# Optimization experiments

Hardware: AMD Instinct MI355X
Metric: run time of the kernel (lower is better)

## Reference

```python
import jax, jax.numpy as jnp
import numpy as np

B, N, D, H, T = 2048, 128, 256, 8, 64
HD = D // H
TANH_C = 10.0
MASK_PENALTY = 1e9


def setup_inputs() -> dict:
    key = jax.random.key(0)
    ks = jax.random.split(key, 16)
    s = 1.0 / np.sqrt(D).astype(np.float32)
    w = lambda k: jax.random.normal(k, (D, D), jnp.float32) * s
    return {
        'node_emb': jax.random.normal(ks[0], (B, N, D), jnp.float32),
        'graph_emb': jax.random.normal(ks[1], (B, D), jnp.float32),
        'W_target': w(ks[2]), 'W_global': w(ks[3]),
        'W_K1': w(ks[4]), 'W_K2': w(ks[5]),
        'W_Q': w(ks[6]), 'W_V': w(ks[7]),
        'Wq_m': w(ks[8]), 'Wk_m': w(ks[9]), 'Wv_m': w(ks[10]), 'Wo_m': w(ks[11]),
        'targets': jax.random.randint(ks[12], (T, B), 0, N, jnp.int32),
        'masks': jax.random.randint(ks[13], (T, B, N), 0, 2, jnp.int32),
    }


def _mha(q, k, v, Wq, Wk, Wv, Wo):
    # q: [B,1,D]; k,v: [B,N,D]. Standard multi-head attention (glimpse).
    qh = (q @ Wq.T).reshape(B, 1, H, HD).transpose(0, 2, 1, 3)   # [B,H,1,HD]
    kh = (k @ Wk.T).reshape(B, N, H, HD).transpose(0, 2, 1, 3)   # [B,H,N,HD]
    vh = (v @ Wv.T).reshape(B, N, H, HD).transpose(0, 2, 1, 3)
    scores = jnp.einsum('bhqd,bhnd->bhqn', qh, kh) / np.sqrt(HD).astype(np.float32)
    attn = jax.nn.softmax(scores, axis=-1)
    out = jnp.einsum('bhqn,bhnd->bhqd', attn, vh)                # [B,H,1,HD]
    out = out.transpose(0, 2, 1, 3).reshape(B, 1, D)
    return out @ Wo.T


def reference(node_emb, graph_emb, W_target, W_global, W_K1, W_K2, W_Q, W_V,
              Wq_m, Wk_m, Wv_m, Wo_m, targets, masks):
    # Step-invariant projections (embeddings fixed across decode steps here).
    keys = node_emb @ W_K1.T      # [B,N,D]
    vals = node_emb @ W_V.T       # [B,N,D]
    key2 = node_emb @ W_K2.T      # [B,N,D]
    g_ctx = graph_emb @ W_global.T  # [B,D]
    inv_sqrt_d = np.float32(1.0 / np.sqrt(D))

    def step(ll, tm):
        tgt, mask = tm  # tgt:[B] int32, mask:[B,N] int32
        tgt_emb = jnp.take_along_axis(node_emb, tgt[:, None, None], axis=1)[:, 0, :]  # [B,D]
        context = (tgt_emb @ W_target.T + g_ctx)[:, None, :]      # [B,1,D]
        glimpse = _mha(context, keys, vals, Wq_m, Wk_m, Wv_m, Wo_m)  # [B,1,D]
        query = glimpse @ W_Q.T                                    # [B,1,D]
        logits = jnp.einsum('bqd,bnd->bn', query, key2) * inv_sqrt_d  # [B,N]
        logits = TANH_C * jnp.tanh(logits) - mask.astype(jnp.float32) * MASK_PENALTY
        log_p = jax.nn.log_softmax(logits, axis=1)
        actions = jnp.argmax(log_p, axis=1)                        # greedy TopKSampler
        ll = ll + jnp.take_along_axis(log_p, actions[:, None], axis=1)[:, 0]
        return ll, None

    ll, _ = jax.lax.scan(step, jnp.zeros(B, jnp.float32), (targets, masks))
    return ll
```

## Files before the change

kernel.cpp:

```cpp
#include <hip/hip_runtime.h>
#include <hip/hip_bf16.h>

#define BB 2048
#define NN 128
#define DD 256
#define HH 8
#define TT 64

typedef __bf16 bf16x8 __attribute__((ext_vector_type(8)));
typedef float f32x4 __attribute__((ext_vector_type(4)));

static __device__ __forceinline__ f32x4 mfma16(bf16x8 a, bf16x8 b, f32x4 c) {
  return __builtin_amdgcn_mfma_f32_16x16x32_bf16(a, b, c, 0, 0, 0);
}

static __device__ __forceinline__ f32x4 zero4() {
  f32x4 z = {0.f, 0.f, 0.f, 0.f};
  return z;
}

static __device__ __forceinline__ bf16x8 cvt8(const float* p) {
  const float4 x0 = *(const float4*)p;
  const float4 x1 = *(const float4*)(p + 4);
  bf16x8 r;
  r[0] = (__bf16)x0.x; r[1] = (__bf16)x0.y; r[2] = (__bf16)x0.z; r[3] = (__bf16)x0.w;
  r[4] = (__bf16)x1.x; r[5] = (__bf16)x1.y; r[6] = (__bf16)x1.z; r[7] = (__bf16)x1.w;
  return r;
}

__global__ void fold1(const float* __restrict__ Wq_m, const float* __restrict__ W_target,
                      const float* __restrict__ W_global, const float* __restrict__ Wk_m,
                      const float* __restrict__ W_K1, const float* __restrict__ Wv_m,
                      const float* __restrict__ W_V, const float* __restrict__ W_Q,
                      const float* __restrict__ Wo_m,
                      __bf16* __restrict__ WTQ, float* __restrict__ WGQT,
                      __bf16* __restrict__ WKH, __bf16* __restrict__ WVH,
                      float* __restrict__ WQO) {
  const int p = blockIdx.x >> 8;
  const int i = blockIdx.x & 255;
  const int t = threadIdx.x;
  __shared__ float arow[256];
  const float* A;
  const float* Bm;
  if (p == 0)      { A = Wq_m; Bm = W_target; }
  else if (p == 1) { A = Wq_m; Bm = W_global; }
  else if (p == 2) { A = Wk_m; Bm = W_K1; }
  else if (p == 3) { A = Wv_m; Bm = W_V; }
  else             { A = W_Q;  Bm = Wo_m; }
  arow[t] = A[i * 256 + t];
  __syncthreads();
  float acc = 0.f;
  for (int k = 0; k < 256; ++k) acc = fmaf(arow[k], Bm[k * 256 + t], acc);
  if (p == 0)      WTQ[i * 256 + t] = (__bf16)acc;
  else if (p == 1) WGQT[t * 256 + i] = acc;
  else if (p == 2) WKH[i * 256 + t] = (__bf16)acc;
  else if (p == 3) WVH[i * 256 + t] = (__bf16)acc;
  else             WQO[i * 256 + t] = acc;
}

__global__ void fold2(const float* __restrict__ WQO, const float* __restrict__ W_K2,
                      __bf16* __restrict__ WZL) {
  const int j = blockIdx.x;
  const int t = threadIdx.x;
  __shared__ float col[256];
  col[t] = W_K2[t * 256 + j];
  __syncthreads();
  float acc = 0.f;
  for (int d = 0; d < 256; ++d) acc = fmaf(WQO[d * 256 + t], col[d], acc);
  WZL[j * 256 + t] = (__bf16)acc;
}

__global__ void gq_kernel(const float* __restrict__ ge, const float* __restrict__ WGQT,
                          float* __restrict__ GQ) {
  const int b = blockIdx.x;
  const int t = threadIdx.x;
  __shared__ float g[256];
  g[t] = ge[b * 256 + t];
  __syncthreads();
  float acc = 0.f;
  for (int j = 0; j < 256; ++j) acc = fmaf(WGQT[j * 256 + t], g[j], acc);
  GQ[b * 256 + t] = acc;
}

__global__ __launch_bounds__(256, 2)
void glimpse_kernel(const float* __restrict__ E, const int* __restrict__ tg,
                    const __bf16* __restrict__ WTQ, const __bf16* __restrict__ WKH,
                    const __bf16* __restrict__ WVH, const float* __restrict__ GQ,
                    __bf16* __restrict__ HO) {
  const int b = blockIdx.x;
  const int tid = threadIdx.x;
  const int w = tid >> 6;
  const int l = tid & 63;
  const int lr = l & 15;
  const int lg = l >> 4;

  __shared__ __bf16 Qs[64 * 264];
  __shared__ __bf16 KHs[128 * 40];
  __shared__ __bf16 VTs[32 * 136];
  __shared__ __bf16 Ps[64 * 136];
  __shared__ int tgs[64];

  if (tid < 64) tgs[tid] = tg[tid * BB + b];
  __syncthreads();

  const float* Eb = E + (size_t)b * NN * DD;

  {
    f32x4 acc[4][4];
#pragma unroll
    for (int mf = 0; mf < 4; ++mf)
#pragma unroll
      for (int nf = 0; nf < 4; ++nf) acc[mf][nf] = zero4();
    const int n0 = w * 64;
    for (int kk = 0; kk < 8; ++kk) {
      bf16x8 aF[4], bF[4];
#pragma unroll
      for (int mf = 0; mf < 4; ++mf) {
        const int node = tgs[mf * 16 + lr];
        aF[mf] = cvt8(Eb + node * DD + kk * 32 + lg * 8);
      }
#pragma unroll
      for (int nf = 0; nf < 4; ++nf)
        bF[nf] = *(const bf16x8*)(WTQ + (size_t)(n0 + nf * 16 + lr) * DD + kk * 32 + lg * 8);
#pragma unroll
      for (int mf = 0; mf < 4; ++mf)
#pragma unroll
        for (int nf = 0; nf < 4; ++nf) acc[mf][nf] = mfma16(aF[mf], bF[nf], acc[mf][nf]);
    }
#pragma unroll
    for (int nf = 0; nf < 4; ++nf) {
      const int col = n0 + nf * 16 + lr;
      const float g = GQ[b * DD + col];
#pragma unroll
      for (int mf = 0; mf < 4; ++mf)
#pragma unroll
        for (int r = 0; r < 4; ++r)
          Qs[(mf * 16 + lg * 4 + r) * 264 + col] = (__bf16)(acc[mf][nf][r] + g);
    }
  }

  for (int h = 0; h < HH; ++h) {
    __syncthreads();
    {
      f32x4 ak[2][2], av[2][2];
#pragma unroll
      for (int mf = 0; mf < 2; ++mf)
#pragma unroll
        for (int nf = 0; nf < 2; ++nf) { ak[mf][nf] = zero4(); av[mf][nf] = zero4(); }
      for (int kk = 0; kk < 8; ++kk) {
        bf16x8 aF[2], bK[2], bV[2];
#pragma unroll
        for (int mf = 0; mf < 2; ++mf)
          aF[mf] = cvt8(Eb + (w * 32 + mf * 16 + lr) * DD + kk * 32 + lg * 8);
#pragma unroll
        for (int nf = 0; nf < 2; ++nf) {
          const size_t wo = (size_t)(h * 32 + nf * 16 + lr) * DD + kk * 32 + lg * 8;
          bK[nf] = *(const bf16x8*)(WKH + wo);
          bV[nf] = *(const bf16x8*)(WVH + wo);
        }
#pragma unroll
        for (int mf = 0; mf < 2; ++mf)
#pragma unroll
          for (int nf = 0; nf < 2; ++nf) {
            ak[mf][nf] = mfma16(aF[mf], bK[nf], ak[mf][nf]);
            av[mf][nf] = mfma16(aF[mf], bV[nf], av[mf][nf]);
          }
      }
#pragma unroll
      for (int mf = 0; mf < 2; ++mf)
#pragma unroll
        for (int nf = 0; nf < 2; ++nf)
#pragma unroll
          for (int r = 0; r < 4; ++r) {
            const int node = w * 32 + mf * 16 + lg * 4 + r;
            const int d = nf * 16 + lr;
            KHs[node * 40 + d] = (__bf16)ak[mf][nf][r];
            VTs[d * 136 + node] = (__bf16)av[mf][nf][r];
          }
    }
    __syncthreads();
    {
      const bf16x8 aq = *(const bf16x8*)&Qs[(w * 16 + lr) * 264 + h * 32 + lg * 8];
      f32x4 s[8];
#pragma unroll
      for (int nf = 0; nf < 8; ++nf)
        s[nf] = mfma16(aq, *(const bf16x8*)&KHs[(nf * 16 + lr) * 40 + lg * 8], zero4());

      float mx[4] = {-1e30f, -1e30f, -1e30f, -1e30f};
#pragma unroll
      for (int nf = 0; nf < 8; ++nf)
#pragma unroll
        for (int r = 0; r < 4; ++r) mx[r] = fmaxf(mx[r], s[nf][r]);
#pragma unroll
      for (int mk = 1; mk <= 8; mk <<= 1)
#pragma unroll
        for (int r = 0; r < 4; ++r) mx[r] = fmaxf(mx[r], __shfl_xor(mx[r], mk));

      float ev[8][4];
      float sm[4] = {0.f, 0.f, 0.f, 0.f};
#pragma unroll
      for (int nf = 0; nf < 8; ++nf)
#pragma unroll
        for (int r = 0; r < 4; ++r) {
          ev[nf][r] = __expf((s[nf][r] - mx[r]) * 0.17677669529663687f);
          sm[r] += ev[nf][r];
        }
#pragma unroll
      for (int mk = 1; mk <= 8; mk <<= 1)
#pragma unroll
        for (int r = 0; r < 4; ++r) sm[r] += __shfl_xor(sm[r], mk);

#pragma unroll
      for (int nf = 0; nf < 8; ++nf)
#pragma unroll
        for (int r = 0; r < 4; ++r)
          Ps[(w * 16 + lg * 4 + r) * 136 + nf * 16 + lr] = (__bf16)ev[nf][r];

      f32x4 o[2] = {zero4(), zero4()};
#pragma unroll
      for (int kk = 0; kk < 4; ++kk) {
        const bf16x8 ap = *(const bf16x8*)&Ps[(w * 16 + lr) * 136 + kk * 32 + lg * 8];
#pragma unroll
        for (int nf2 = 0; nf2 < 2; ++nf2)
          o[nf2] = mfma16(ap, *(const bf16x8*)&VTs[(nf2 * 16 + lr) * 136 + kk * 32 + lg * 8],
                          o[nf2]);
      }
      float inv[4];
#pragma unroll
      for (int r = 0; r < 4; ++r) inv[r] = 1.f / sm[r];
#pragma unroll
      for (int nf2 = 0; nf2 < 2; ++nf2)
#pragma unroll
        for (int r = 0; r < 4; ++r) {
          const int t = w * 16 + lg * 4 + r;
          HO[((size_t)t * BB + b) * DD + h * 32 + nf2 * 16 + lr] =
              (__bf16)(o[nf2][r] * inv[r]);
        }
    }
  }
}

__global__ __launch_bounds__(256, 2)
void logits_kernel(const float* __restrict__ E, const __bf16* __restrict__ HO,
                   const __bf16* __restrict__ WZL, const int* __restrict__ MK,
                   float* __restrict__ out) {
  const int b = blockIdx.x;
  const int tid = threadIdx.x;
  const int w = tid >> 6;
  const int l = tid & 63;
  const int lr = l & 15;
  const int lg = l >> 4;

  __shared__ __bf16 HOs[64 * 264];
  __shared__ __bf16 Zs[64 * 264];
  __shared__ float red[4];

#pragma unroll
  for (int it = 0; it < 8; ++it) {
    const int lin = it * 256 + tid;
    const int tr = lin >> 5;
    const int c8 = lin & 31;
    *(bf16x8*)&HOs[tr * 264 + c8 * 8] =
        *(const bf16x8*)(HO + ((size_t)tr * BB + b) * DD + c8 * 8);
  }
  __syncthreads();

  {
    f32x4 acc[4][4];
#pragma unroll
    for (int mf = 0; mf < 4; ++mf)
#pragma unroll
      for (int nf = 0; nf < 4; ++nf) acc[mf][nf] = zero4();
    for (int kk = 0; kk < 8; ++kk) {
      bf16x8 aF[4], bF[4];
#pragma unroll
      for (int mf = 0; mf < 4; ++mf)
        aF[mf] = *(const bf16x8*)&HOs[(mf * 16 + lr) * 264 + kk * 32 + lg * 8];
#pragma unroll
      for (int nf = 0; nf < 4; ++nf)
        bF[nf] = *(const bf16x8*)(WZL + (size_t)(w * 64 + nf * 16 + lr) * DD + kk * 32 + lg * 8);
#pragma unroll
      for (int mf = 0; mf < 4; ++mf)
#pragma unroll
        for (int nf = 0; nf < 4; ++nf) acc[mf][nf] = mfma16(aF[mf], bF[nf], acc[mf][nf]);
    }
#pragma unroll
    for (int mf = 0; mf < 4; ++mf)
#pragma unroll
      for (int nf = 0; nf < 4; ++nf)
#pragma unroll
        for (int r = 0; r < 4; ++r)
          Zs[(mf * 16 + lg * 4 + r) * 264 + w * 64 + nf * 16 + lr] = (__bf16)acc[mf][nf][r];
  }
  __syncthreads();

  {
    const float* Eb = E + (size_t)b * NN * DD;
    f32x4 sa[8];
#pragma unroll
    for (int nf = 0; nf < 8; ++nf) sa[nf] = zero4();
    for (int kk = 0; kk < 8; ++kk) {
      const bf16x8 az = *(const bf16x8*)&Zs[(w * 16 + lr) * 264 + kk * 32 + lg * 8];
#pragma unroll
      for (int nf = 0; nf < 8; ++nf) {
        const bf16x8 be = cvt8(Eb + (nf * 16 + lr) * DD + kk * 32 + lg * 8);
        sa[nf] = mfma16(az, be, sa[nf]);
      }
    }
    float xv[8][4];
    float mx[4] = {-3e38f, -3e38f, -3e38f, -3e38f};
    float sm[4] = {0.f, 0.f, 0.f, 0.f};
#pragma unroll
    for (int nf = 0; nf < 8; ++nf)
#pragma unroll
      for (int r = 0; r < 4; ++r) {
        const int t = w * 16 + lg * 4 + r;
        const int n = nf * 16 + lr;
        const int m = MK[((size_t)t * BB + b) * NN + n];
        const float x = 10.f * tanhf(sa[nf][r] * 0.0625f) - (float)m * 1e9f;
        xv[nf][r] = x;
        mx[r] = fmaxf(mx[r], x);
      }
#pragma unroll
    for (int mk = 1; mk <= 8; mk <<= 1)
#pragma unroll
      for (int r = 0; r < 4; ++r) mx[r] = fmaxf(mx[r], __shfl_xor(mx[r], mk));
#pragma unroll
    for (int nf = 0; nf < 8; ++nf)
#pragma unroll
      for (int r = 0; r < 4; ++r) sm[r] += __expf(xv[nf][r] - mx[r]);
#pragma unroll
    for (int mk = 1; mk <= 8; mk <<= 1)
#pragma unroll
      for (int r = 0; r < 4; ++r) sm[r] += __shfl_xor(sm[r], mk);

    float part = logf(sm[0]) + logf(sm[1]) + logf(sm[2]) + logf(sm[3]);
    part += __shfl_xor(part, 16);
    part += __shfl_xor(part, 32);
    if (l == 0) red[w] = part;
  }
  __syncthreads();
  if (tid == 0) out[b] = -(red[0] + red[1] + red[2] + red[3]);
}

extern "C" void kernel_launch(void* const* d_in, const int* in_sizes, int n_in,
                              void* d_out, int out_size, void* d_ws, size_t ws_size,
                              hipStream_t stream) {
  (void)in_sizes; (void)n_in; (void)out_size; (void)ws_size;
  const float* node_emb  = (const float*)d_in[0];
  const float* graph_emb = (const float*)d_in[1];
  const float* W_target  = (const float*)d_in[2];
  const float* W_global  = (const float*)d_in[3];
  const float* W_K1      = (const float*)d_in[4];
  const float* W_K2      = (const float*)d_in[5];
  const float* W_Q       = (const float*)d_in[6];
  const float* W_V       = (const float*)d_in[7];
  const float* Wq_m      = (const float*)d_in[8];
  const float* Wk_m      = (const float*)d_in[9];
  const float* Wv_m      = (const float*)d_in[10];
  const float* Wo_m      = (const float*)d_in[11];
  const int* targets     = (const int*)d_in[12];
  const int* masks       = (const int*)d_in[13];

  char* p = (char*)d_ws;
  __bf16* HO  = (__bf16*)p; p += (size_t)TT * BB * DD * 2;
  __bf16* WTQ = (__bf16*)p; p += 256 * 256 * 2;
  __bf16* WKH = (__bf16*)p; p += 256 * 256 * 2;
  __bf16* WVH = (__bf16*)p; p += 256 * 256 * 2;
  __bf16* WZL = (__bf16*)p; p += 256 * 256 * 2;
  float* WGQT = (float*)p;  p += 256 * 256 * 4;
  float* WQO  = (float*)p;  p += 256 * 256 * 4;
  float* GQ   = (float*)p;  p += (size_t)BB * DD * 4;

  fold1<<<1280, 256, 0, stream>>>(Wq_m, W_target, W_global, Wk_m, W_K1, Wv_m, W_V, W_Q, Wo_m,
                                  WTQ, WGQT, WKH, WVH, WQO);
  fold2<<<256, 256, 0, stream>>>(WQO, W_K2, WZL);
  gq_kernel<<<BB, 256, 0, stream>>>(graph_emb, WGQT, GQ);
  glimpse_kernel<<<BB, 256, 0, stream>>>(node_emb, targets, WTQ, WKH, WVH, GQ, HO);
  logits_kernel<<<BB, 256, 0, stream>>>(node_emb, HO, WZL, masks, (float*)d_out);
}
```

Baseline: 616.5 us.

## Split glimpse kernel across head pairs and use fast tanh in logits

The glimpse kernel now launches four blocks per batch element, each handling two heads (64 columns). Each block computes its slice of Q, K and V in one pass and drops the per-head sync loop. This raises parallelism and shrinks shared memory per block. The cost is that the node embedding rows are loaded and converted four times per batch element instead of once. Separately, tanhf in the logits kernel is replaced by an exp/rcp formula, which is cheaper but slightly less accurate.

```diff
diff --git a/kernel.cpp b/kernel.cpp
--- a/kernel.cpp
+++ b/kernel.cpp
@@ -26,6 +26,11 @@
   r[0] = (__bf16)x0.x; r[1] = (__bf16)x0.y; r[2] = (__bf16)x0.z; r[3] = (__bf16)x0.w;
   r[4] = (__bf16)x1.x; r[5] = (__bf16)x1.y; r[6] = (__bf16)x1.z; r[7] = (__bf16)x1.w;
   return r;
+}
+
+static __device__ __forceinline__ float fast_tanh10(float y) {
+  const float e = __expf(2.f * y);
+  return 10.f - 20.f * __builtin_amdgcn_rcpf(1.f + e);
 }
 
 __global__ void fold1(const float* __restrict__ Wq_m, const float* __restrict__ W_target,
@@ -83,20 +88,21 @@
 }
 
 __global__ __launch_bounds__(256, 2)
-void glimpse_kernel(const float* __restrict__ E, const int* __restrict__ tg,
-                    const __bf16* __restrict__ WTQ, const __bf16* __restrict__ WKH,
-                    const __bf16* __restrict__ WVH, const float* __restrict__ GQ,
-                    __bf16* __restrict__ HO) {
-  const int b = blockIdx.x;
+void glimpse2_kernel(const float* __restrict__ E, const int* __restrict__ tg,
+                     const __bf16* __restrict__ WTQ, const __bf16* __restrict__ WKH,
+                     const __bf16* __restrict__ WVH, const float* __restrict__ GQ,
+                     __bf16* __restrict__ HO) {
+  const int b = blockIdx.x >> 2;
+  const int c0 = (blockIdx.x & 3) * 64;
   const int tid = threadIdx.x;
   const int w = tid >> 6;
   const int l = tid & 63;
   const int lr = l & 15;
   const int lg = l >> 4;
 
-  __shared__ __bf16 Qs[64 * 264];
-  __shared__ __bf16 KHs[128 * 40];
-  __shared__ __bf16 VTs[32 * 136];
+  __shared__ __bf16 Qs[64 * 72];
+  __shared__ __bf16 KHs[128 * 72];
+  __shared__ __bf16 VTs[64 * 136];
   __shared__ __bf16 Ps[64 * 136];
   __shared__ int tgs[64];
 
@@ -106,137 +112,123 @@
   const float* Eb = E + (size_t)b * NN * DD;
 
   {
-    f32x4 acc[4][4];
-#pragma unroll
-    for (int mf = 0; mf < 4; ++mf)
-#pragma unroll
-      for (int nf = 0; nf < 4; ++nf) acc[mf][nf] = zero4();
-    const int n0 = w * 64;
+    f32x4 acc[4] = {zero4(), zero4(), zero4(), zero4()};
+    const int node = tgs[w * 16 + lr];
     for (int kk = 0; kk < 8; ++kk) {
-      bf16x8 aF[4], bF[4];
-#pragma unroll
-      for (int mf = 0; mf < 4; ++mf) {
-        const int node = tgs[mf * 16 + lr];
-        aF[mf] = cvt8(Eb + node * DD + kk * 32 + lg * 8);
-      }
-#pragma unroll
-      for (int nf = 0; nf < 4; ++nf)
-        bF[nf] = *(const bf16x8*)(WTQ + (size_t)(n0 + nf * 16 + lr) * DD + kk * 32 + lg * 8);
-#pragma unroll
-      for (int mf = 0; mf < 4; ++mf)
-#pragma unroll
-        for (int nf = 0; nf < 4; ++nf) acc[mf][nf] = mfma16(aF[mf], bF[nf], acc[mf][nf]);
+      const bf16x8 aF = cvt8(Eb + node * DD + kk * 32 + lg * 8);
+#pragma unroll
+      for (int nf = 0; nf < 4; ++nf) {
+        const bf16x8 bF =
+            *(const bf16x8*)(WTQ + (size_t)(c0 + nf * 16 + lr) * DD + kk * 32 + lg * 8);
+        acc[nf] = mfma16(aF, bF, acc[nf]);
+      }
     }
 #pragma unroll
     for (int nf = 0; nf < 4; ++nf) {
-      const int col = n0 + nf * 16 + lr;
-      const float g = GQ[b * DD + col];
-#pragma unroll
-      for (int mf = 0; mf < 4; ++mf)
-#pragma unroll
-        for (int r = 0; r < 4; ++r)
-          Qs[(mf * 16 + lg * 4 + r) * 264 + col] = (__bf16)(acc[mf][nf][r] + g);
-    }
-  }
-
-  for (int h = 0; h < HH; ++h) {
-    __syncthreads();
-    {
-      f32x4 ak[2][2], av[2][2];
+      const int cl = nf * 16 + lr;
+      const float g = GQ[b * DD + c0 + cl];
+#pragma unroll
+      for (int r = 0; r < 4; ++r)
+        Qs[(w * 16 + lg * 4 + r) * 72 + cl] = (__bf16)(acc[nf][r] + g);
+    }
+  }
+
+  {
+    f32x4 acc[2][8];
+#pragma unroll
+    for (int mf = 0; mf < 2; ++mf)
+#pragma unroll
+      for (int nf = 0; nf < 8; ++nf) acc[mf][nf] = zero4();
+    for (int kk = 0; kk < 8; ++kk) {
+      bf16x8 aF[2], bF[8];
 #pragma unroll
       for (int mf = 0; mf < 2; ++mf)
-#pragma unroll
-        for (int nf = 0; nf < 2; ++nf) { ak[mf][nf] = zero4(); av[mf][nf] = zero4(); }
-      for (int kk = 0; kk < 8; ++kk) {
-        bf16x8 aF[2], bK[2], bV[2];
-#pragma unroll
-        for (int mf = 0; mf < 2; ++mf)
-          aF[mf] = cvt8(Eb + (w * 32 + mf * 16 + lr) * DD + kk * 32 + lg * 8);
-#pragma unroll
-        for (int nf = 0; nf < 2; ++nf) {
-          const size_t wo = (size_t)(h * 32 + nf * 16 + lr) * DD + kk * 32 + lg * 8;
-          bK[nf] = *(const bf16x8*)(WKH + wo);
-          bV[nf] = *(const bf16x8*)(WVH + wo);
-        }
-#pragma unroll
-        for (int mf = 0; mf < 2; ++mf)
-#pragma unroll
-          for (int nf = 0; nf < 2; ++nf) {
-            ak[mf][nf] = mfma16(aF[mf], bK[nf], ak[mf][nf]);
-            av[mf][nf] = mfma16(aF[mf], bV[nf], av[mf][nf]);
-          }
+        aF[mf] = cvt8(Eb + (w * 32 + mf * 16 + lr) * DD + kk * 32 + lg * 8);
+#pragma unroll
+      for (int nf = 0; nf < 4; ++nf) {
+        const size_t wo = (size_t)(c0 + nf * 16 + lr) * DD + kk * 32 + lg * 8;
+        bF[nf] = *(const bf16x8*)(WKH + wo);
+        bF[nf + 4] = *(const bf16x8*)(WVH + wo);
       }
 #pragma unroll
       for (int mf = 0; mf < 2; ++mf)
 #pragma unroll
-        for (int nf = 0; nf < 2; ++nf)
-#pragma unroll
-          for (int r = 0; r < 4; ++r) {
-            const int node = w * 32 + mf * 16 + lg * 4 + r;
-            const int d = nf * 16 + lr;
-            KHs[node * 40 + d] = (__bf16)ak[mf][nf][r];
-            VTs[d * 136 + node] = (__bf16)av[mf][nf][r];
-          }
-    }
-    __syncthreads();
-    {
-      const bf16x8 aq = *(const bf16x8*)&Qs[(w * 16 + lr) * 264 + h * 32 + lg * 8];
-      f32x4 s[8];
-#pragma unroll
-      for (int nf = 0; nf < 8; ++nf)
-        s[nf] = mfma16(aq, *(const bf16x8*)&KHs[(nf * 16 + lr) * 40 + lg * 8], zero4());
-
-      float mx[4] = {-1e30f, -1e30f, -1e30f, -1e30f};
-#pragma unroll
-      for (int nf = 0; nf < 8; ++nf)
-#pragma unroll
-        for (int r = 0; r < 4; ++r) mx[r] = fmaxf(mx[r], s[nf][r]);
-#pragma unroll
-      for (int mk = 1; mk <= 8; mk <<= 1)
-#pragma unroll
-        for (int r = 0; r < 4; ++r) mx[r] = fmaxf(mx[r], __shfl_xor(mx[r], mk));
-
-      float ev[8][4];
-      float sm[4] = {0.f, 0.f, 0.f, 0.f};
-#pragma unroll
-      for (int nf = 0; nf < 8; ++nf)
-#pragma unroll
-        for (int r = 0; r < 4; ++r) {
-          ev[nf][r] = __expf((s[nf][r] - mx[r]) * 0.17677669529663687f);
-          sm[r] += ev[nf][r];
-        }
-#pragma unroll
-      for (int mk = 1; mk <= 8; mk <<= 1)
-#pragma unroll
-        for (int r = 0; r < 4; ++r) sm[r] += __shfl_xor(sm[r], mk);
-
-#pragma unroll
-      for (int nf = 0; nf < 8; ++nf)
-#pragma unroll
-        for (int r = 0; r < 4; ++r)
-          Ps[(w * 16 + lg * 4 + r) * 136 + nf * 16 + lr] = (__bf16)ev[nf][r];
-
-      f32x4 o[2] = {zero4(), zero4()};
-#pragma unroll
-      for (int kk = 0; kk < 4; ++kk) {
-        const bf16x8 ap = *(const bf16x8*)&Ps[(w * 16 + lr) * 136 + kk * 32 + lg * 8];
-#pragma unroll
-        for (int nf2 = 0; nf2 < 2; ++nf2)
-          o[nf2] = mfma16(ap, *(const bf16x8*)&VTs[(nf2 * 16 + lr) * 136 + kk * 32 + lg * 8],
-                          o[nf2]);
-      }
-      float inv[4];
-#pragma unroll
-      for (int r = 0; r < 4; ++r) inv[r] = 1.f / sm[r];
+        for (int nf = 0; nf < 8; ++nf) acc[mf][nf] = mfma16(aF[mf], bF[nf], acc[mf][nf]);
+    }
+#pragma unroll
+    for (int mf = 0; mf < 2; ++mf)
+#pragma unroll
+      for (int r = 0; r < 4; ++r) {
+        const int node = w * 32 + mf * 16 + lg * 4 + r;
+#pragma unroll
+        for (int nf = 0; nf < 4; ++nf)
+          KHs[node * 72 + nf * 16 + lr] = (__bf16)acc[mf][nf][r];
+#pragma unroll
+        for (int nf = 0; nf < 4; ++nf)
+          VTs[(nf * 16 + lr) * 136 + node] = (__bf16)acc[mf][nf + 4][r];
+      }
+  }
+  __syncthreads();
+
+#pragma unroll
+  for (int h = 0; h < 2; ++h) {
+    const bf16x8 aq = *(const bf16x8*)&Qs[(w * 16 + lr) * 72 + h * 32 + lg * 8];
+    f32x4 s[8];
+#pragma unroll
+    for (int nf = 0; nf < 8; ++nf)
+      s[nf] = mfma16(aq, *(const bf16x8*)&KHs[(nf * 16 + lr) * 72 + h * 32 + lg * 8], zero4());
+
+    float mx[4] = {-1e30f, -1e30f, -1e30f, -1e30f};
+#pragma unroll
+    for (int nf = 0; nf < 8; ++nf)
+#pragma unroll
+      for (int r = 0; r < 4; ++r) mx[r] = fmaxf(mx[r], s[nf][r]);
+#pragma unroll
+    for (int mk = 1; mk <= 8; mk <<= 1)
+#pragma unroll
+      for (int r = 0; r < 4; ++r) mx[r] = fmaxf(mx[r], __shfl_xor(mx[r], mk));
+
+    float ev[8][4];
+    float sm[4] = {0.f, 0.f, 0.f, 0.f};
+#pragma unroll
+    for (int nf = 0; nf < 8; ++nf)
+#pragma unroll
+      for (int r = 0; r < 4; ++r) {
+        ev[nf][r] = __expf((s[nf][r] - mx[r]) * 0.17677669529663687f);
+        sm[r] += ev[nf][r];
+      }
+#pragma unroll
+    for (int mk = 1; mk <= 8; mk <<= 1)
+#pragma unroll
+      for (int r = 0; r < 4; ++r) sm[r] += __shfl_xor(sm[r], mk);
+
+#pragma unroll
+    for (int nf = 0; nf < 8; ++nf)
+#pragma unroll
+      for (int r = 0; r < 4; ++r)
+        Ps[(w * 16 + lg * 4 + r) * 136 + nf * 16 + lr] = (__bf16)ev[nf][r];
+
+    f32x4 o[2] = {zero4(), zero4()};
+#pragma unroll
+    for (int kk = 0; kk < 4; ++kk) {
+      const bf16x8 ap = *(const bf16x8*)&Ps[(w * 16 + lr) * 136 + kk * 32 + lg * 8];
 #pragma unroll
       for (int nf2 = 0; nf2 < 2; ++nf2)
-#pragma unroll
-        for (int r = 0; r < 4; ++r) {
-          const int t = w * 16 + lg * 4 + r;
-          HO[((size_t)t * BB + b) * DD + h * 32 + nf2 * 16 + lr] =
-              (__bf16)(o[nf2][r] * inv[r]);
-        }
-    }
+        o[nf2] = mfma16(
+            ap, *(const bf16x8*)&VTs[(h * 32 + nf2 * 16 + lr) * 136 + kk * 32 + lg * 8],
+            o[nf2]);
+    }
+    float inv[4];
+#pragma unroll
+    for (int r = 0; r < 4; ++r) inv[r] = 1.f / sm[r];
+#pragma unroll
+    for (int nf2 = 0; nf2 < 2; ++nf2)
+#pragma unroll
+      for (int r = 0; r < 4; ++r) {
+        const int t = w * 16 + lg * 4 + r;
+        HO[((size_t)t * BB + b) * DD + c0 + h * 32 + nf2 * 16 + lr] =
+            (__bf16)(o[nf2][r] * inv[r]);
+      }
   }
 }
 
@@ -317,7 +309,7 @@
         const int t = w * 16 + lg * 4 + r;
         const int n = nf * 16 + lr;
         const int m = MK[((size_t)t * BB + b) * NN + n];
-        const float x = 10.f * tanhf(sa[nf][r] * 0.0625f) - (float)m * 1e9f;
+        const float x = fast_tanh10(sa[nf][r] * 0.0625f) - (float)m * 1e9f;
         xv[nf][r] = x;
         mx[r] = fmaxf(mx[r], x);
       }
@@ -376,6 +368,6 @@
                                   WTQ, WGQT, WKH, WVH, WQO);
   fold2<<<256, 256, 0, stream>>>(WQO, W_K2, WZL);
   gq_kernel<<<BB, 256, 0, stream>>>(graph_emb, WGQT, GQ);
-  glimpse_kernel<<<BB, 256, 0, stream>>>(node_emb, targets, WTQ, WKH, WVH, GQ, HO);
+  glimpse2_kernel<<<BB * 4, 256, 0, stream>>>(node_emb, targets, WTQ, WKH, WVH, GQ, HO);
   logits_kernel<<<BB, 256, 0, stream>>>(node_emb, HO, WZL, masks, (float*)d_out);
 }
```

Measured after the change: 751.9 us. 1.22x slower.

## Split K/V projection into its own kernel and fuse attention with logits

Applied to the files above, without the earlier changes.

Moves the per-batch key/value head projections into a separate kernel. It stages node embeddings in LDS as bf16 once and writes K and V-transposed for all heads to global memory. The attention and logits stages merge into one kernel that reads K and V from global and keeps head outputs in LDS and registers, so the large HO intermediate round trip goes away. It also replaces tanhf with an exp plus reciprocal formulation. The cost is writing and reading KH and VT (two B×N×D bf16 buffers), a larger LDS tile in the KV kernel that may lower occupancy, and slightly different tanh accuracy.

```diff
diff --git a/kernel.cpp b/kernel.cpp
--- a/kernel.cpp
+++ b/kernel.cpp
@@ -26,6 +26,11 @@
   r[0] = (__bf16)x0.x; r[1] = (__bf16)x0.y; r[2] = (__bf16)x0.z; r[3] = (__bf16)x0.w;
   r[4] = (__bf16)x1.x; r[5] = (__bf16)x1.y; r[6] = (__bf16)x1.z; r[7] = (__bf16)x1.w;
   return r;
+}
+
+static __device__ __forceinline__ float fast_tanh10(float y) {
+  const float e = __expf(2.f * y);
+  return 10.f - 20.f * __builtin_amdgcn_rcpf(1.f + e);
 }
 
 __global__ void fold1(const float* __restrict__ Wq_m, const float* __restrict__ W_target,
@@ -82,168 +87,90 @@
   GQ[b * 256 + t] = acc;
 }
 
-__global__ __launch_bounds__(256, 2)
-void glimpse_kernel(const float* __restrict__ E, const int* __restrict__ tg,
-                    const __bf16* __restrict__ WTQ, const __bf16* __restrict__ WKH,
-                    const __bf16* __restrict__ WVH, const float* __restrict__ GQ,
-                    __bf16* __restrict__ HO) {
+__global__ __launch_bounds__(256)
+void kv_kernel(const float* __restrict__ E, const __bf16* __restrict__ WKH,
+               const __bf16* __restrict__ WVH, __bf16* __restrict__ KH,
+               __bf16* __restrict__ VT) {
   const int b = blockIdx.x;
   const int tid = threadIdx.x;
   const int w = tid >> 6;
   const int l = tid & 63;
   const int lr = l & 15;
   const int lg = l >> 4;
-
-  __shared__ __bf16 Qs[64 * 264];
-  __shared__ __bf16 KHs[128 * 40];
-  __shared__ __bf16 VTs[32 * 136];
-  __shared__ __bf16 Ps[64 * 136];
-  __shared__ int tgs[64];
-
-  if (tid < 64) tgs[tid] = tg[tid * BB + b];
-  __syncthreads();
-
+  __shared__ __bf16 Es[128 * 264];
   const float* Eb = E + (size_t)b * NN * DD;
-
-  {
-    f32x4 acc[4][4];
+  for (int c = tid; c < 4096; c += 256) {
+    const int row = c >> 5;
+    const int c8 = c & 31;
+    *(bf16x8*)&Es[row * 264 + c8 * 8] = cvt8(Eb + row * 256 + c8 * 8);
+  }
+  __syncthreads();
+
+  {
+    f32x4 acc[8][4];
+#pragma unroll
+    for (int mf = 0; mf < 8; ++mf)
+#pragma unroll
+      for (int nf = 0; nf < 4; ++nf) acc[mf][nf] = zero4();
+    for (int kk = 0; kk < 8; ++kk) {
+      bf16x8 aF[8], bF[4];
+#pragma unroll
+      for (int mf = 0; mf < 8; ++mf)
+        aF[mf] = *(const bf16x8*)&Es[(mf * 16 + lr) * 264 + kk * 32 + lg * 8];
+#pragma unroll
+      for (int nf = 0; nf < 4; ++nf)
+        bF[nf] = *(const bf16x8*)(WKH + (size_t)(w * 64 + nf * 16 + lr) * DD + kk * 32 + lg * 8);
+#pragma unroll
+      for (int mf = 0; mf < 8; ++mf)
+#pragma unroll
+        for (int nf = 0; nf < 4; ++nf) acc[mf][nf] = mfma16(aF[mf], bF[nf], acc[mf][nf]);
+    }
+    __bf16* KHb = KH + (size_t)b * NN * DD;
+#pragma unroll
+    for (int mf = 0; mf < 8; ++mf)
+#pragma unroll
+      for (int nf = 0; nf < 4; ++nf)
+#pragma unroll
+        for (int r = 0; r < 4; ++r)
+          KHb[(mf * 16 + lg * 4 + r) * DD + w * 64 + nf * 16 + lr] = (__bf16)acc[mf][nf][r];
+  }
+
+  {
+    f32x4 acc[4][8];
 #pragma unroll
     for (int mf = 0; mf < 4; ++mf)
 #pragma unroll
-      for (int nf = 0; nf < 4; ++nf) acc[mf][nf] = zero4();
-    const int n0 = w * 64;
-    for (int kk = 0; kk < 8; ++kk) {
-      bf16x8 aF[4], bF[4];
-#pragma unroll
-      for (int mf = 0; mf < 4; ++mf) {
-        const int node = tgs[mf * 16 + lr];
-        aF[mf] = cvt8(Eb + node * DD + kk * 32 + lg * 8);
-      }
-#pragma unroll
-      for (int nf = 0; nf < 4; ++nf)
-        bF[nf] = *(const bf16x8*)(WTQ + (size_t)(n0 + nf * 16 + lr) * DD + kk * 32 + lg * 8);
-#pragma unroll
-      for (int mf = 0; mf < 4; ++mf)
-#pragma unroll
-        for (int nf = 0; nf < 4; ++nf) acc[mf][nf] = mfma16(aF[mf], bF[nf], acc[mf][nf]);
-    }
-#pragma unroll
-    for (int nf = 0; nf < 4; ++nf) {
-      const int col = n0 + nf * 16 + lr;
-      const float g = GQ[b * DD + col];
-#pragma unroll
-      for (int mf = 0; mf < 4; ++mf)
+      for (int nf = 0; nf < 8; ++nf) acc[mf][nf] = zero4();
+    for (int kk = 0; kk < 8; ++kk) {
+      bf16x8 aF[4], bF[8];
+#pragma unroll
+      for (int mf = 0; mf < 4; ++mf)
+        aF[mf] = *(const bf16x8*)(WVH + (size_t)(w * 64 + mf * 16 + lr) * DD + kk * 32 + lg * 8);
+#pragma unroll
+      for (int nf = 0; nf < 8; ++nf)
+        bF[nf] = *(const bf16x8*)&Es[(nf * 16 + lr) * 264 + kk * 32 + lg * 8];
+#pragma unroll
+      for (int mf = 0; mf < 4; ++mf)
+#pragma unroll
+        for (int nf = 0; nf < 8; ++nf) acc[mf][nf] = mfma16(aF[mf], bF[nf], acc[mf][nf]);
+    }
+    __bf16* VTb = VT + (size_t)b * DD * NN;
+#pragma unroll
+    for (int mf = 0; mf < 4; ++mf)
+#pragma unroll
+      for (int nf = 0; nf < 8; ++nf)
 #pragma unroll
         for (int r = 0; r < 4; ++r)
-          Qs[(mf * 16 + lg * 4 + r) * 264 + col] = (__bf16)(acc[mf][nf][r] + g);
-    }
-  }
-
-  for (int h = 0; h < HH; ++h) {
-    __syncthreads();
-    {
-      f32x4 ak[2][2], av[2][2];
-#pragma unroll
-      for (int mf = 0; mf < 2; ++mf)
-#pragma unroll
-        for (int nf = 0; nf < 2; ++nf) { ak[mf][nf] = zero4(); av[mf][nf] = zero4(); }
-      for (int kk = 0; kk < 8; ++kk) {
-        bf16x8 aF[2], bK[2], bV[2];
-#pragma unroll
-        for (int mf = 0; mf < 2; ++mf)
-          aF[mf] = cvt8(Eb + (w * 32 + mf * 16 + lr) * DD + kk * 32 + lg * 8);
-#pragma unroll
-        for (int nf = 0; nf < 2; ++nf) {
-          const size_t wo = (size_t)(h * 32 + nf * 16 + lr) * DD + kk * 32 + lg * 8;
-          bK[nf] = *(const bf16x8*)(WKH + wo);
-          bV[nf] = *(const bf16x8*)(WVH + wo);
-        }
-#pragma unroll
-        for (int mf = 0; mf < 2; ++mf)
-#pragma unroll
-          for (int nf = 0; nf < 2; ++nf) {
-            ak[mf][nf] = mfma16(aF[mf], bK[nf], ak[mf][nf]);
-            av[mf][nf] = mfma16(aF[mf], bV[nf], av[mf][nf]);
-          }
-      }
-#pragma unroll
-      for (int mf = 0; mf < 2; ++mf)
-#pragma unroll
-        for (int nf = 0; nf < 2; ++nf)
-#pragma unroll
-          for (int r = 0; r < 4; ++r) {
-            const int node = w * 32 + mf * 16 + lg * 4 + r;
-            const int d = nf * 16 + lr;
-            KHs[node * 40 + d] = (__bf16)ak[mf][nf][r];
-            VTs[d * 136 + node] = (__bf16)av[mf][nf][r];
-          }
-    }
-    __syncthreads();
-    {
-      const bf16x8 aq = *(const bf16x8*)&Qs[(w * 16 + lr) * 264 + h * 32 + lg * 8];
-      f32x4 s[8];
-#pragma unroll
-      for (int nf = 0; nf < 8; ++nf)
-        s[nf] = mfma16(aq, *(const bf16x8*)&KHs[(nf * 16 + lr) * 40 + lg * 8], zero4());
-
-      float mx[4] = {-1e30f, -1e30f, -1e30f, -1e30f};
-#pragma unroll
-      for (int nf = 0; nf < 8; ++nf)
-#pragma unroll
-        for (int r = 0; r < 4; ++r) mx[r] = fmaxf(mx[r], s[nf][r]);
-#pragma unroll
-      for (int mk = 1; mk <= 8; mk <<= 1)
-#pragma unroll
-        for (int r = 0; r < 4; ++r) mx[r] = fmaxf(mx[r], __shfl_xor(mx[r], mk));
-
-      float ev[8][4];
-      float sm[4] = {0.f, 0.f, 0.f, 0.f};
-#pragma unroll
-      for (int nf = 0; nf < 8; ++nf)
-#pragma unroll
-        for (int r = 0; r < 4; ++r) {
-          ev[nf][r] = __expf((s[nf][r] - mx[r]) * 0.17677669529663687f);
-          sm[r] += ev[nf][r];
-        }
-#pragma unroll
-      for (int mk = 1; mk <= 8; mk <<= 1)
-#pragma unroll
-        for (int r = 0; r < 4; ++r) sm[r] += __shfl_xor(sm[r], mk);
-
-#pragma unroll
-      for (int nf = 0; nf < 8; ++nf)
-#pragma unroll
-        for (int r = 0; r < 4; ++r)
-          Ps[(w * 16 + lg * 4 + r) * 136 + nf * 16 + lr] = (__bf16)ev[nf][r];
-
-      f32x4 o[2] = {zero4(), zero4()};
-#pragma unroll
-      for (int kk = 0; kk < 4; ++kk) {
-        const bf16x8 ap = *(const bf16x8*)&Ps[(w * 16 + lr) * 136 + kk * 32 + lg * 8];
-#pragma unroll
-        for (int nf2 = 0; nf2 < 2; ++nf2)
-          o[nf2] = mfma16(ap, *(const bf16x8*)&VTs[(nf2 * 16 + lr) * 136 + kk * 32 + lg * 8],
-                          o[nf2]);
-      }
-      float inv[4];
-#pragma unroll
-      for (int r = 0; r < 4; ++r) inv[r] = 1.f / sm[r];
-#pragma unroll
-      for (int nf2 = 0; nf2 < 2; ++nf2)
-#pragma unroll
-        for (int r = 0; r < 4; ++r) {
-          const int t = w * 16 + lg * 4 + r;
-          HO[((size_t)t * BB + b) * DD + h * 32 + nf2 * 16 + lr] =
-              (__bf16)(o[nf2][r] * inv[r]);
-        }
-    }
-  }
-}
-
-__global__ __launch_bounds__(256, 2)
-void logits_kernel(const float* __restrict__ E, const __bf16* __restrict__ HO,
-                   const __bf16* __restrict__ WZL, const int* __restrict__ MK,
-                   float* __restrict__ out) {
+          VTb[(w * 64 + mf * 16 + lg * 4 + r) * NN + nf * 16 + lr] = (__bf16)acc[mf][nf][r];
+  }
+}
+
+__global__ __launch_bounds__(256)
+void attn_logits_kernel(const float* __restrict__ E, const int* __restrict__ tg,
+                        const __bf16* __restrict__ WTQ, const float* __restrict__ GQ,
+                        const __bf16* __restrict__ KH, const __bf16* __restrict__ VT,
+                        const __bf16* __restrict__ WZL, const int* __restrict__ MK,
+                        float* __restrict__ out) {
   const int b = blockIdx.x;
   const int tid = threadIdx.x;
   const int w = tid >> 6;
@@ -251,59 +178,134 @@
   const int lr = l & 15;
   const int lg = l >> 4;
 
-  __shared__ __bf16 HOs[64 * 264];
-  __shared__ __bf16 Zs[64 * 264];
+  __shared__ __bf16 Qs[64 * 264];
+  __shared__ __bf16 Ps[64 * 136];
   __shared__ float red[4];
 
-#pragma unroll
-  for (int it = 0; it < 8; ++it) {
-    const int lin = it * 256 + tid;
-    const int tr = lin >> 5;
-    const int c8 = lin & 31;
-    *(bf16x8*)&HOs[tr * 264 + c8 * 8] =
-        *(const bf16x8*)(HO + ((size_t)tr * BB + b) * DD + c8 * 8);
-  }
-  __syncthreads();
-
-  {
-    f32x4 acc[4][4];
+  const float* Eb = E + (size_t)b * NN * DD;
+
+  {
+    f32x4 qa[4][4];
 #pragma unroll
     for (int mf = 0; mf < 4; ++mf)
 #pragma unroll
-      for (int nf = 0; nf < 4; ++nf) acc[mf][nf] = zero4();
+      for (int nf = 0; nf < 4; ++nf) qa[mf][nf] = zero4();
+    const int n0 = w * 64;
+    int nd[4];
+#pragma unroll
+    for (int mf = 0; mf < 4; ++mf) nd[mf] = tg[(mf * 16 + lr) * BB + b];
     for (int kk = 0; kk < 8; ++kk) {
       bf16x8 aF[4], bF[4];
 #pragma unroll
       for (int mf = 0; mf < 4; ++mf)
-        aF[mf] = *(const bf16x8*)&HOs[(mf * 16 + lr) * 264 + kk * 32 + lg * 8];
+        aF[mf] = cvt8(Eb + (size_t)nd[mf] * DD + kk * 32 + lg * 8);
 #pragma unroll
       for (int nf = 0; nf < 4; ++nf)
-        bF[nf] = *(const bf16x8*)(WZL + (size_t)(w * 64 + nf * 16 + lr) * DD + kk * 32 + lg * 8);
-#pragma unroll
-      for (int mf = 0; mf < 4; ++mf)
-#pragma unroll
-        for (int nf = 0; nf < 4; ++nf) acc[mf][nf] = mfma16(aF[mf], bF[nf], acc[mf][nf]);
-    }
-#pragma unroll
-    for (int mf = 0; mf < 4; ++mf)
-#pragma unroll
-      for (int nf = 0; nf < 4; ++nf)
+        bF[nf] = *(const bf16x8*)(WTQ + (size_t)(n0 + nf * 16 + lr) * DD + kk * 32 + lg * 8);
+#pragma unroll
+      for (int mf = 0; mf < 4; ++mf)
+#pragma unroll
+        for (int nf = 0; nf < 4; ++nf) qa[mf][nf] = mfma16(aF[mf], bF[nf], qa[mf][nf]);
+    }
+#pragma unroll
+    for (int nf = 0; nf < 4; ++nf) {
+      const int col = n0 + nf * 16 + lr;
+      const float g = GQ[b * DD + col];
+#pragma unroll
+      for (int mf = 0; mf < 4; ++mf)
 #pragma unroll
         for (int r = 0; r < 4; ++r)
-          Zs[(mf * 16 + lg * 4 + r) * 264 + w * 64 + nf * 16 + lr] = (__bf16)acc[mf][nf][r];
-  }
-  __syncthreads();
-
-  {
-    const float* Eb = E + (size_t)b * NN * DD;
+          Qs[(mf * 16 + lg * 4 + r) * 264 + col] = (__bf16)(qa[mf][nf][r] + g);
+    }
+  }
+  __syncthreads();
+
+  const __bf16* KHb = KH + (size_t)b * NN * DD;
+  const __bf16* VTb = VT + (size_t)b * DD * NN;
+  f32x4 hov[16];
+
+#pragma unroll
+  for (int h = 0; h < HH; ++h) {
+    const bf16x8 aq = *(const bf16x8*)&Qs[(w * 16 + lr) * 264 + h * 32 + lg * 8];
+    f32x4 s[8];
+#pragma unroll
+    for (int nf = 0; nf < 8; ++nf)
+      s[nf] = mfma16(aq, *(const bf16x8*)(KHb + (size_t)(nf * 16 + lr) * DD + h * 32 + lg * 8),
+                     zero4());
+
+    float mx[4] = {-1e30f, -1e30f, -1e30f, -1e30f};
+#pragma unroll
+    for (int nf = 0; nf < 8; ++nf)
+#pragma unroll
+      for (int r = 0; r < 4; ++r) mx[r] = fmaxf(mx[r], s[nf][r]);
+#pragma unroll
+    for (int mk = 1; mk <= 8; mk <<= 1)
+#pragma unroll
+      for (int r = 0; r < 4; ++r) mx[r] = fmaxf(mx[r], __shfl_xor(mx[r], mk));
+
+    float sm[4] = {0.f, 0.f, 0.f, 0.f};
+#pragma unroll
+    for (int nf = 0; nf < 8; ++nf)
+#pragma unroll
+      for (int r = 0; r < 4; ++r) {
+        const float e = __expf((s[nf][r] - mx[r]) * 0.17677669529663687f);
+        sm[r] += e;
+        Ps[(w * 16 + lg * 4 + r) * 136 + nf * 16 + lr] = (__bf16)e;
+      }
+#pragma unroll
+    for (int mk = 1; mk <= 8; mk <<= 1)
+#pragma unroll
+      for (int r = 0; r < 4; ++r) sm[r] += __shfl_xor(sm[r], mk);
+
+    f32x4 o0 = zero4(), o1 = zero4();
+#pragma unroll
+    for (int kk = 0; kk < 4; ++kk) {
+      const bf16x8 ap = *(const bf16x8*)&Ps[(w * 16 + lr) * 136 + kk * 32 + lg * 8];
+      o0 = mfma16(ap, *(const bf16x8*)(VTb + (size_t)(h * 32 + lr) * NN + kk * 32 + lg * 8), o0);
+      o1 = mfma16(ap, *(const bf16x8*)(VTb + (size_t)(h * 32 + 16 + lr) * NN + kk * 32 + lg * 8),
+                  o1);
+    }
+#pragma unroll
+    for (int r = 0; r < 4; ++r) {
+      const float inv = 1.f / sm[r];
+      hov[h * 2][r] = o0[r] * inv;
+      hov[h * 2 + 1][r] = o1[r] * inv;
+    }
+  }
+
+  {
+#pragma unroll
+    for (int i = 0; i < 16; ++i)
+#pragma unroll
+      for (int r = 0; r < 4; ++r)
+        Qs[(w * 16 + lg * 4 + r) * 264 + (i >> 1) * 32 + (i & 1) * 16 + lr] = (__bf16)hov[i][r];
+
+    f32x4 za[16];
+#pragma unroll
+    for (int nf = 0; nf < 16; ++nf) za[nf] = zero4();
+    for (int kk = 0; kk < 8; ++kk) {
+      const bf16x8 aF = *(const bf16x8*)&Qs[(w * 16 + lr) * 264 + kk * 32 + lg * 8];
+#pragma unroll
+      for (int nf = 0; nf < 16; ++nf)
+        za[nf] = mfma16(aF, *(const bf16x8*)(WZL + (size_t)(nf * 16 + lr) * DD + kk * 32 + lg * 8),
+                        za[nf]);
+    }
+#pragma unroll
+    for (int nf = 0; nf < 16; ++nf)
+#pragma unroll
+      for (int r = 0; r < 4; ++r)
+        Qs[(w * 16 + lg * 4 + r) * 264 + nf * 16 + lr] = (__bf16)za[nf][r];
+  }
+
+  {
     f32x4 sa[8];
 #pragma unroll
     for (int nf = 0; nf < 8; ++nf) sa[nf] = zero4();
     for (int kk = 0; kk < 8; ++kk) {
-      const bf16x8 az = *(const bf16x8*)&Zs[(w * 16 + lr) * 264 + kk * 32 + lg * 8];
+      const bf16x8 az = *(const bf16x8*)&Qs[(w * 16 + lr) * 264 + kk * 32 + lg * 8];
 #pragma unroll
       for (int nf = 0; nf < 8; ++nf) {
-        const bf16x8 be = cvt8(Eb + (nf * 16 + lr) * DD + kk * 32 + lg * 8);
+        const bf16x8 be = cvt8(Eb + (size_t)(nf * 16 + lr) * DD + kk * 32 + lg * 8);
         sa[nf] = mfma16(az, be, sa[nf]);
       }
     }
@@ -317,7 +319,7 @@
         const int t = w * 16 + lg * 4 + r;
         const int n = nf * 16 + lr;
         const int m = MK[((size_t)t * BB + b) * NN + n];
-        const float x = 10.f * tanhf(sa[nf][r] * 0.0625f) - (float)m * 1e9f;
+        const float x = fast_tanh10(sa[nf][r] * 0.0625f) - (float)m * 1e9f;
         xv[nf][r] = x;
         mx[r] = fmaxf(mx[r], x);
       }
@@ -363,7 +365,8 @@
   const int* masks       = (const int*)d_in[13];
 
   char* p = (char*)d_ws;
-  __bf16* HO  = (__bf16*)p; p += (size_t)TT * BB * DD * 2;
+  __bf16* KH  = (__bf16*)p; p += (size_t)BB * NN * DD * 2;
+  __bf16* VT  = (__bf16*)p; p += (size_t)BB * DD * NN * 2;
   __bf16* WTQ = (__bf16*)p; p += 256 * 256 * 2;
   __bf16* WKH = (__bf16*)p; p += 256 * 256 * 2;
   __bf16* WVH = (__bf16*)p; p += 256 * 256 * 2;
@@ -376,6 +379,7 @@
                                   WTQ, WGQT, WKH, WVH, WQO);
   fold2<<<256, 256, 0, stream>>>(WQO, W_K2, WZL);
   gq_kernel<<<BB, 256, 0, stream>>>(graph_emb, WGQT, GQ);
-  glimpse_kernel<<<BB, 256, 0, stream>>>(node_emb, targets, WTQ, WKH, WVH, GQ, HO);
-  logits_kernel<<<BB, 256, 0, stream>>>(node_emb, HO, WZL, masks, (float*)d_out);
-}
+  kv_kernel<<<BB, 256, 0, stream>>>(node_emb, WKH, WVH, KH, VT);
+  attn_logits_kernel<<<BB, 256, 0, stream>>>(node_emb, targets, WTQ, GQ, KH, VT, WZL, masks,
+                                             (float*)d_out);
+}
```

Result: slower. 686.4 us (+11.3%).
